# Kernel optimization log

Hardware: AMD Instinct MI355X
Metric: run time of the kernel (lower is better)

The kernel has to match this reference:

```python
import jax, jax.numpy as jnp
import numpy as np

B, A, D, H, NL, DFF, V, NB = 32, 256, 512, 8, 6, 2048, 1000, 4
EMB = D // 8  # per-subtoken embedding dim, 8 subtokens concat to d_model


def setup_inputs() -> dict:
    key = jax.random.key(0)
    ks = jax.random.split(key, 10)
    s = 0.02
    p = {}
    p["src"] = jax.random.randint(ks[0], (B, A, 8), 0, V, dtype=jnp.int32)
    p["mask"] = jnp.ones((B, 1, A), dtype=bool)
    p["max_atoms"] = A
    # sinusoidal positional encoding table [A, D]
    pos = np.arange(A, dtype=np.float32)[:, None]
    div = np.power(10000.0, np.arange(0, D, 2, dtype=np.float32) / D)
    pe = np.zeros((A, D), dtype=np.float32)
    pe[:, 0::2] = np.sin(pos / div)
    pe[:, 1::2] = np.cos(pos / div)
    p["pe"] = jnp.asarray(pe)
    p["embed"] = s * jax.random.normal(ks[1], (V, EMB), dtype=jnp.float32)
    p["Wq"] = s * jax.random.normal(ks[2], (NL, D, D), dtype=jnp.float32)
    p["Wk"] = s * jax.random.normal(ks[3], (NL, D, D), dtype=jnp.float32)
    p["Wv"] = s * jax.random.normal(ks[4], (NL, D, D), dtype=jnp.float32)
    p["Wo"] = s * jax.random.normal(ks[5], (NL, D, D), dtype=jnp.float32)
    p["W1"] = s * jax.random.normal(ks[6], (NL, D, DFF), dtype=jnp.float32)
    p["W2"] = s * jax.random.normal(ks[7], (NL, DFF, D), dtype=jnp.float32)
    p["Wfl"] = s * jax.random.normal(ks[8], (2 * D, NB), dtype=jnp.float32)
    for n, sh in [("bq", (NL, D)), ("bk", (NL, D)), ("bv", (NL, D)), ("bo", (NL, D)),
                  ("b1", (NL, DFF)), ("b2", (NL, D)), ("ln1_b", (NL, D)), ("ln2_b", (NL, D)),
                  ("fn_b", (D,)), ("bfl", (NB,))]:
        p[n] = jnp.zeros(sh, dtype=jnp.float32)
    for n, sh in [("ln1_a", (NL, D)), ("ln2_a", (NL, D)), ("fn_a", (D,))]:
        p[n] = jnp.ones(sh, dtype=jnp.float32)
    return p


def _norm(x, a, b):
    # custom Norm: alpha * (x - mean) / (std_unbiased + eps) + bias
    mu = x.mean(-1, keepdims=True)
    sd = jnp.std(x, axis=-1, ddof=1, keepdims=True)
    return a * (x - mu) / (sd + 1e-6) + b


def _forward(src, mask, max_atoms, embed, pe, Wq, bq, Wk, bk, Wv, bv, Wo, bo,
             ln1_a, ln1_b, ln2_a, ln2_b, W1, b1, W2, b2, fn_a, fn_b, Wfl, bfl):
    b, L = src.shape[0], src.shape[1]
    x = embed[src].reshape(b, L, -1)  # [B, A, D]
    d = x.shape[-1]
    x = x * jnp.sqrt(jnp.float32(d)) + pe[None, :L]
    dk = d // H
    addm = jnp.where(mask[:, None, :, :], 0.0, -1e9)  # [B,1,1,A]
    for i in range(NL):
        # pre-norm self-attention + residual
        x2 = _norm(x, ln1_a[i], ln1_b[i])
        q = (x2 @ Wq[i] + bq[i]).reshape(b, L, H, dk)
        k = (x2 @ Wk[i] + bk[i]).reshape(b, L, H, dk)
        v = (x2 @ Wv[i] + bv[i]).reshape(b, L, H, dk)
        sc = jnp.einsum('bqhd,bkhd->bhqk', q, k) / jnp.sqrt(jnp.float32(dk)) + addm
        att = jax.nn.softmax(sc, axis=-1)
        o = jnp.einsum('bhqk,bkhd->bqhd', att, v).reshape(b, L, d)
        x = x + (o @ Wo[i] + bo[i])
        # pre-norm FFN + residual
        x2 = _norm(x, ln2_a[i], ln2_b[i])
        x = x + (jax.nn.relu(x2 @ W1[i] + b1[i]) @ W2[i] + b2[i])
    h = _norm(x, fn_a, fn_b)  # [B, A, D]
    # EdgeClassify: all-pairs concat(h_i, h_j) @ Wfl + bfl, computed without
    # materializing the [B, A, A, 2D] tensor (linearity of the Linear layer)
    left = h @ Wfl[:d]    # [B, A, NB]
    right = h @ Wfl[d:]   # [B, A, NB]
    return left[:, :, None, :] + right[:, None, :, :] + bfl  # [B, A, A, NB]


def reference(src, mask, max_atoms, pe, embed, Wq, Wk, Wv, Wo, W1, W2, Wfl,
              bq, bk, bv, bo, b1, b2, ln1_b, ln2_b, fn_b, bfl, ln1_a, ln2_a, fn_a):
    return _forward(src, mask, max_atoms, embed, pe, Wq, bq, Wk, bk, Wv, bv, Wo, bo,
                    ln1_a, ln1_b, ln2_a, ln2_b, W1, b1, W2, b2, fn_a, fn_b, Wfl, bfl)
```

## Files before the change

kernel.cpp:

```cpp
#include <hip/hip_runtime.h>
#include <hip/hip_bf16.h>
#include <type_traits>

#define BB 32
#define AA 256
#define DD 512
#define HH 8
#define NLAYER 6
#define DFF 2048
#define NB 4

typedef float  f32x4_t  __attribute__((ext_vector_type(4)));
typedef short  bf16x8_t __attribute__((ext_vector_type(8)));

struct __align__(16) US8 { ushort u[8]; };

__device__ __forceinline__ ushort f2bf(float f) {
    __hip_bfloat16 h = __float2bfloat16(f);
    return *reinterpret_cast<ushort*>(&h);
}
__device__ __forceinline__ float bf2f(ushort u) {
    __hip_bfloat16 h;
    *reinterpret_cast<ushort*>(&h) = u;
    return __bfloat162float(h);
}

__device__ __forceinline__ void gload16(const void* g, void* l) {
    __builtin_amdgcn_global_load_lds(
        (const __attribute__((address_space(1))) void*)g,
        (__attribute__((address_space(3))) void*)l, 16, 0, 0);
}

template<int N> __device__ __forceinline__ void wait_vmcnt() {
    if constexpr      (N == 0)  asm volatile("s_waitcnt vmcnt(0)"  ::: "memory");
    else if constexpr (N == 3)  asm volatile("s_waitcnt vmcnt(3)"  ::: "memory");
    else if constexpr (N == 4)  asm volatile("s_waitcnt vmcnt(4)"  ::: "memory");
    else static_assert(N == 0, "add vmcnt literal");
}
template<int N> using ic = std::integral_constant<int, N>;

__global__ __launch_bounds__(256) void embed_pe_kernel(
    const int* __restrict__ src, const float* __restrict__ embed,
    const float* __restrict__ pe, float* __restrict__ x)
{
    int t = blockIdx.x * 256 + threadIdx.x;
    int d4 = t & 127;
    int row = t >> 7;
    int a = row & 255;
    int d = d4 * 4;
    int sub = d >> 6;
    int e = d & 63;
    int tok = src[row * 8 + sub];
    float4 em = *(const float4*)&embed[tok * 64 + e];
    float4 p  = *(const float4*)&pe[a * DD + d];
    const float s = 22.627416997969522f;
    float4 r;
    r.x = em.x * s + p.x; r.y = em.y * s + p.y;
    r.z = em.z * s + p.z; r.w = em.w * s + p.w;
    *(float4*)&x[(long long)row * DD + d] = r;
}

template<bool OB>
__global__ __launch_bounds__(256) void layernorm512_kernel(
    const float* x, const float* __restrict__ alpha,
    const float* __restrict__ beta, void* yv)
{
    const int row = blockIdx.x * 4 + (threadIdx.x >> 6);
    const int lane = threadIdx.x & 63;
    const float* xr = x + (long long)row * DD;
    float4 v0 = *(const float4*)&xr[lane * 8];
    float4 v1 = *(const float4*)&xr[lane * 8 + 4];
    float s  = v0.x + v0.y + v0.z + v0.w + v1.x + v1.y + v1.z + v1.w;
    float ss = v0.x*v0.x + v0.y*v0.y + v0.z*v0.z + v0.w*v0.w
             + v1.x*v1.x + v1.y*v1.y + v1.z*v1.z + v1.w*v1.w;
    #pragma unroll
    for (int off = 1; off < 64; off <<= 1) {
        s  += __shfl_xor(s, off, 64);
        ss += __shfl_xor(ss, off, 64);
    }
    float mu = s * (1.0f / 512.0f);
    float var = fmaxf(ss - 512.0f * mu * mu, 0.0f) * (1.0f / 511.0f);
    float inv = 1.0f / (sqrtf(var) + 1e-6f);
    float4 a0 = *(const float4*)&alpha[lane * 8];
    float4 a1 = *(const float4*)&alpha[lane * 8 + 4];
    float4 b0 = *(const float4*)&beta[lane * 8];
    float4 b1 = *(const float4*)&beta[lane * 8 + 4];
    float o0 = a0.x * (v0.x - mu) * inv + b0.x;
    float o1 = a0.y * (v0.y - mu) * inv + b0.y;
    float o2 = a0.z * (v0.z - mu) * inv + b0.z;
    float o3 = a0.w * (v0.w - mu) * inv + b0.w;
    float o4 = a1.x * (v1.x - mu) * inv + b1.x;
    float o5 = a1.y * (v1.y - mu) * inv + b1.y;
    float o6 = a1.z * (v1.z - mu) * inv + b1.z;
    float o7 = a1.w * (v1.w - mu) * inv + b1.w;
    if (OB) {
        US8 o;
        o.u[0] = f2bf(o0); o.u[1] = f2bf(o1); o.u[2] = f2bf(o2); o.u[3] = f2bf(o3);
        o.u[4] = f2bf(o4); o.u[5] = f2bf(o5); o.u[6] = f2bf(o6); o.u[7] = f2bf(o7);
        *(US8*)((ushort*)yv + (long long)row * DD + lane * 8) = o;
    } else {
        float* yr = (float*)yv + (long long)row * DD + lane * 8;
        float4 w0 = {o0, o1, o2, o3}, w1 = {o4, o5, o6, o7};
        *(float4*)yr = w0;
        *(float4*)(yr + 4) = w1;
    }
}

__global__ __launch_bounds__(256) void wtrans_kernel(
    const float* __restrict__ src, ushort* __restrict__ dst,
    int Nsz, int Ksz, long long sSrc, long long sDst)
{
    __shared__ float tile[64][65];
    src += blockIdx.z * sSrc;
    dst += blockIdx.z * sDst;
    const int n0 = blockIdx.x * 64, k0 = blockIdx.y * 64;
    const int t = threadIdx.x, col = t & 63, r4 = t >> 6;
    #pragma unroll
    for (int p = 0; p < 16; ++p) {
        int row = p * 4 + r4;
        tile[row][col] = src[(long long)(k0 + row) * Nsz + n0 + col];
    }
    __syncthreads();
    #pragma unroll
    for (int p = 0; p < 16; ++p) {
        int row = p * 4 + r4;
        dst[(long long)(n0 + row) * Ksz + k0 + col] = f2bf(tile[col][row]);
    }
}

__global__ __launch_bounds__(256) void vtrans_kernel(
    const ushort* __restrict__ qkv, ushort* __restrict__ vT)
{
    __shared__ ushort tile[64][65];
    const int b = blockIdx.z;
    const int c0 = blockIdx.x * 64, a0 = blockIdx.y * 64;
    const int t = threadIdx.x, col = t & 63, r4 = t >> 6;
    const ushort* src = qkv + (long long)b * 256 * 1536 + 1024;
    ushort* dst = vT + (long long)b * 512 * 256;
    #pragma unroll
    for (int p = 0; p < 16; ++p) {
        int row = p * 4 + r4;
        tile[row][col] = src[(long long)(a0 + row) * 1536 + c0 + col];
    }
    __syncthreads();
    #pragma unroll
    for (int p = 0; p < 16; ++p) {
        int row = p * 4 + r4;
        dst[(long long)(c0 + row) * 256 + a0 + col] = tile[col][row];
    }
}

__global__ void concat_bias_kernel(const float* __restrict__ bq,
    const float* __restrict__ bk, const float* __restrict__ bv,
    float* __restrict__ o)
{
    int i = blockIdx.x * 256 + threadIdx.x;
    if (i >= NLAYER * 1536) return;
    int l = i / 1536, r = i % 1536;
    float v = r < 512 ? bq[l * 512 + r]
            : (r < 1024 ? bk[l * 512 + r - 512] : bv[l * 512 + r - 1024]);
    o[i] = v;
}

__global__ __launch_bounds__(512, 1) void attn_kernel(
    const ushort* __restrict__ qkv, const ushort* __restrict__ vT,
    ushort* __restrict__ Ob)
{
    __shared__ ushort Kl[256 * 64];
    __shared__ ushort Vl[64 * 256];
    __shared__ ushort Pl[8 * 16 * 256];

    const int t = threadIdx.x;
    const int bh = blockIdx.x;
    const int b = bh >> 3, h = bh & 7;
    const int w = t >> 6, lane = t & 63;
    const int lr = lane & 15, lg = lane >> 4;

    {
        const int j = t >> 3, slot = t & 7;
        const int chunk = slot ^ (j & 7);
        const ushort* srcK = qkv + (long long)(b * 256 + j) * 1536 + 512 + h * 64 + chunk * 8;
        const int c = t >> 5, slv = t & 31;
        const int chv = slv ^ (c & 7);
        const ushort* srcV = vT + (long long)b * 131072 + (long long)(h * 64 + c) * 256 + chv * 8;
        #pragma unroll
        for (int r = 0; r < 4; ++r) {
            gload16(srcK + (long long)r * 64 * 1536, &Kl[(t + r * 512) * 8]);
            gload16(srcV + (long long)r * 16 * 256,  &Vl[(t + r * 512) * 8]);
        }
    }
    asm volatile("s_waitcnt vmcnt(0)" ::: "memory");
    __builtin_amdgcn_sched_barrier(0);
    __builtin_amdgcn_s_barrier();
    __builtin_amdgcn_sched_barrier(0);

    char* Pw = (char*)Pl + w * 8192;
    const char* Kc = (const char*)Kl;
    const char* Vc = (const char*)Vl;

    #pragma unroll 1
    for (int pass = 0; pass < 2; ++pass) {
        const int i0 = pass * 128 + w * 16;
        const ushort* qbase = qkv + (long long)(b * 256 + i0 + lr) * 1536 + h * 64 + lg * 8;
        bf16x8_t qf0 = *(const bf16x8_t*)qbase;
        bf16x8_t qf1 = *(const bf16x8_t*)(qbase + 32);

        f32x4_t s[16];
        #pragma unroll
        for (int jf = 0; jf < 16; ++jf) s[jf] = (f32x4_t){0.f, 0.f, 0.f, 0.f};
        #pragma unroll
        for (int jf = 0; jf < 16; ++jf) {
            const int row = jf * 16 + lr;
            bf16x8_t k0 = *(const bf16x8_t*)(Kc + row * 128 + ((lg ^ (row & 7)) * 16));
            s[jf] = __builtin_amdgcn_mfma_f32_16x16x32_bf16(k0, qf0, s[jf], 0, 0, 0);
        }
        #pragma unroll
        for (int jf = 0; jf < 16; ++jf) {
            const int row = jf * 16 + lr;
            bf16x8_t k1 = *(const bf16x8_t*)(Kc + row * 128 + (((4 + lg) ^ (row & 7)) * 16));
            s[jf] = __builtin_amdgcn_mfma_f32_16x16x32_bf16(k1, qf1, s[jf], 0, 0, 0);
        }

        float m = -3.0e38f;
        #pragma unroll
        for (int jf = 0; jf < 16; ++jf)
            #pragma unroll
            for (int r = 0; r < 4; ++r) m = fmaxf(m, s[jf][r]);
        m = fmaxf(m, __shfl_xor(m, 16, 64));
        m = fmaxf(m, __shfl_xor(m, 32, 64));
        float l = 0.f;
        #pragma unroll
        for (int jf = 0; jf < 16; ++jf)
            #pragma unroll
            for (int r = 0; r < 4; ++r) {
                float e = __expf((s[jf][r] - m) * 0.125f);
                s[jf][r] = e; l += e;
            }
        l += __shfl_xor(l, 16, 64);
        l += __shfl_xor(l, 32, 64);
        const float inv = 1.0f / l;

        #pragma unroll
        for (int jf = 0; jf < 16; ++jf) {
            ushort4 u;
            u.x = f2bf(s[jf][0] * inv); u.y = f2bf(s[jf][1] * inv);
            u.z = f2bf(s[jf][2] * inv); u.w = f2bf(s[jf][3] * inv);
            const int off = (lr * 512 + jf * 32 + lg * 8) ^ ((lr & 7) << 4);
            *(ushort4*)(Pw + off) = u;
        }
        asm volatile("s_waitcnt lgkmcnt(0)" ::: "memory");
        __builtin_amdgcn_sched_barrier(0);

        f32x4_t o[4];
        #pragma unroll
        for (int cf = 0; cf < 4; ++cf) o[cf] = (f32x4_t){0.f, 0.f, 0.f, 0.f};
        #pragma unroll
        for (int ks = 0; ks < 8; ++ks) {
            bf16x8_t pa = *(const bf16x8_t*)(Pw +
                ((lr * 512 + ks * 64 + lg * 16) ^ ((lr & 7) << 4)));
            #pragma unroll
            for (int cf = 0; cf < 4; ++cf) {
                const int crow = cf * 16 + lr;
                bf16x8_t vb = *(const bf16x8_t*)(Vc + crow * 512 +
                    (((ks * 4 + lg) ^ (crow & 7)) * 16));
                o[cf] = __builtin_amdgcn_mfma_f32_16x16x32_bf16(pa, vb, o[cf], 0, 0, 0);
            }
        }
        asm volatile("s_waitcnt lgkmcnt(0)" ::: "memory");
        __builtin_amdgcn_sched_barrier(0);

        #pragma unroll
        for (int cf = 0; cf < 4; ++cf) {
            const int c = cf * 16 + lr;
            #pragma unroll
            for (int r = 0; r < 4; ++r) {
                const int i = i0 + lg * 4 + r;
                Ob[(long long)(b * 256 + i) * 512 + h * 64 + c] = f2bf(o[cf][r]);
            }
        }
    }
}

template<int NT, bool RELU>
__global__ __launch_bounds__(512) void gemm_wide(
    const ushort* __restrict__ A, const ushort* __restrict__ B,
    const float* __restrict__ bias, ushort* __restrict__ C,
    int lda, int ldb, int ldc, int gn)
{
    constexpr int BK = 32;
    constexpr int S = 3;
    __shared__ ushort As[3][256 * BK];
    __shared__ ushort Bs[3][128 * BK];

    const int t = threadIdx.x;
    const int nwg = gridDim.x, bid = blockIdx.x;
    const int swz = (bid & 7) * (nwg >> 3) + (bid >> 3);
    const int nb = swz % gn;
    const int mb = swz / gn;
    const int m0 = mb * 256, n0 = nb * 128;

    const int trow  = t >> 2;
    const int tslot = (t & 3) ^ ((t >> 3) & 3);
    const ushort* Ap = A + (long long)(m0 + trow) * lda + tslot * 8;
    const ushort* Bp = B + (long long)(n0 + trow) * ldb + tslot * 8;

    const int w = t >> 6, lane = t & 63;
    const int wr = w >> 1, wc = w & 1;
    const int lr = lane & 15;
    const int slotK = (((lane >> 4) ^ ((lr >> 1) & 3)) * 8);

    f32x4_t acc[4][4];
    #pragma unroll
    for (int i = 0; i < 4; ++i)
        #pragma unroll
        for (int j = 0; j < 4; ++j)
            acc[i][j] = (f32x4_t){0.f, 0.f, 0.f, 0.f};

    auto stage = [&](int pf) {
        const int buf = pf % 3;
        const long long ko = (long long)pf * BK;
        gload16(Ap + ko,                        &As[buf][t * 8]);
        gload16(Ap + ko + (long long)128 * lda, &As[buf][t * 8 + 4096]);
        gload16(Bp + ko,                        &Bs[buf][t * 8]);
    };

    auto kstep = [&](auto wn, int kt, int pf) {
        wait_vmcnt<decltype(wn)::value>();
        __builtin_amdgcn_sched_barrier(0);
        __builtin_amdgcn_s_barrier();
        __builtin_amdgcn_sched_barrier(0);
        if (pf >= 0) stage(pf);
        __builtin_amdgcn_sched_barrier(0);
        const int cb = kt % 3;
        bf16x8_t af[4], bfr[4];
        #pragma unroll
        for (int mf = 0; mf < 4; ++mf)
            af[mf] = *(const bf16x8_t*)&As[cb][(wr * 64 + mf * 16 + lr) * BK + slotK];
        #pragma unroll
        for (int nf = 0; nf < 4; ++nf)
            bfr[nf] = *(const bf16x8_t*)&Bs[cb][(wc * 64 + nf * 16 + lr) * BK + slotK];
        __builtin_amdgcn_s_setprio(1);
        #pragma unroll
        for (int mf = 0; mf < 4; ++mf)
            #pragma unroll
            for (int nf = 0; nf < 4; ++nf)
                acc[mf][nf] = __builtin_amdgcn_mfma_f32_16x16x32_bf16(
                    af[mf], bfr[nf], acc[mf][nf], 0, 0, 0);
        __builtin_amdgcn_s_setprio(0);
    };

    stage(0);
    stage(1);
    for (int kt = 0; kt < NT - 1; ++kt)
        kstep(ic<S>{}, kt, (kt + 2 < NT) ? (kt + 2) : -1);
    kstep(ic<0>{}, NT - 1, -1);

    #pragma unroll
    for (int nf = 0; nf < 4; ++nf) {
        const int col = n0 + wc * 64 + nf * 16 + lr;
        const float bv = bias[col];
        #pragma unroll
        for (int mf = 0; mf < 4; ++mf) {
            const int row0 = m0 + wr * 64 + mf * 16 + (lane >> 4) * 4;
            #pragma unroll
            for (int j = 0; j < 4; ++j) {
                float vv = acc[mf][nf][j] + bv;
                if (RELU) vv = fmaxf(vv, 0.0f);
                C[(long long)(row0 + j) * ldc + col] = f2bf(vv);
            }
        }
    }
}

template<int BMt, int BNt, int NT, bool OBF16, bool RELU, bool RES, bool SWZ>
__global__ __launch_bounds__(256) void gemm_nar(
    const ushort* __restrict__ A, const ushort* __restrict__ B,
    const float* __restrict__ bias, const float* __restrict__ res,
    void* __restrict__ Cv, int lda, int ldb, int ldc, int gx,
    int zdiv, long long sA1, long long sA2, long long sB1, long long sB2,
    long long sC1, long long sC2)
{
    constexpr int BK = 32;
    constexpr int AI = (BMt * BK) / 2048;
    constexpr int BI = (BNt * BK) / 2048;
    constexpr int S  = AI + BI;
    constexpr int HM = BMt / 2, HN = BNt / 2;
    constexpr int RM = HM / 16, RN = HN / 16;

    __shared__ ushort As[3][BMt * BK];
    __shared__ ushort Bs[3][BNt * BK];

    const int t = threadIdx.x;
    int nb, mb, zq, zr;
    if (SWZ) {
        const int nwg = gridDim.x, bid = blockIdx.x;
        const int swz = (bid & 7) * (nwg >> 3) + (bid >> 3);
        nb = swz % gx; mb = swz / gx; zq = 0; zr = 0;
    } else {
        nb = blockIdx.x; mb = blockIdx.y;
        const int z = blockIdx.z;
        zq = z / zdiv; zr = z % zdiv;
    }
    const int m0 = mb * BMt, n0 = nb * BNt;

    const int trow  = t >> 2;
    const int tslot = (t & 3) ^ ((t >> 3) & 3);
    const ushort* Ap = A + zq * sA1 + zr * sA2
                     + (long long)(m0 + trow) * lda + tslot * 8;
    const ushort* Bp = B + zq * sB1 + zr * sB2
                     + (long long)(n0 + trow) * ldb + tslot * 8;

    const int w = t >> 6, lane = t & 63;
    const int wr = w >> 1, wc = w & 1;
    const int lr = lane & 15;
    const int slotK = (((lane >> 4) ^ ((lr >> 1) & 3)) * 8);

    f32x4_t acc[RM][RN];
    #pragma unroll
    for (int i = 0; i < RM; ++i)
        #pragma unroll
        for (int j = 0; j < RN; ++j)
            acc[i][j] = (f32x4_t){0.f, 0.f, 0.f, 0.f};

    auto stage = [&](int pf) {
        const int buf = pf % 3;
        const long long ko = (long long)pf * BK;
        #pragma unroll
        for (int i = 0; i < AI; ++i)
            gload16(Ap + ko + (long long)i * 64 * lda, &As[buf][t * 8 + i * 2048]);
        #pragma unroll
        for (int i = 0; i < BI; ++i)
            gload16(Bp + ko + (long long)i * 64 * ldb, &Bs[buf][t * 8 + i * 2048]);
    };

    auto kstep = [&](auto wn, int kt, int pf) {
        wait_vmcnt<decltype(wn)::value>();
        __builtin_amdgcn_sched_barrier(0);
        __builtin_amdgcn_s_barrier();
        __builtin_amdgcn_sched_barrier(0);
        if (pf >= 0) stage(pf);
        __builtin_amdgcn_sched_barrier(0);
        const int cb = kt % 3;
        bf16x8_t af[RM], bfr[RN];
        #pragma unroll
        for (int mf = 0; mf < RM; ++mf)
            af[mf] = *(const bf16x8_t*)&As[cb][(wr * HM + mf * 16 + lr) * BK + slotK];
        #pragma unroll
        for (int nf = 0; nf < RN; ++nf)
            bfr[nf] = *(const bf16x8_t*)&Bs[cb][(wc * HN + nf * 16 + lr) * BK + slotK];
        __builtin_amdgcn_s_setprio(1);
        #pragma unroll
        for (int mf = 0; mf < RM; ++mf)
            #pragma unroll
            for (int nf = 0; nf < RN; ++nf)
                acc[mf][nf] = __builtin_amdgcn_mfma_f32_16x16x32_bf16(
                    af[mf], bfr[nf], acc[mf][nf], 0, 0, 0);
        __builtin_amdgcn_s_setprio(0);
    };

    stage(0);
    if constexpr (NT >= 2) stage(1);
    for (int kt = 0; kt < NT - 1; ++kt)
        kstep(ic<S>{}, kt, (kt + 2 < NT) ? (kt + 2) : -1);
    kstep(ic<0>{}, NT - 1, -1);

    const long long coff = zq * sC1 + zr * sC2;
    #pragma unroll
    for (int nf = 0; nf < RN; ++nf) {
        const int col = n0 + wc * HN + nf * 16 + lr;
        const float bv = bias ? bias[col] : 0.0f;
        #pragma unroll
        for (int mf = 0; mf < RM; ++mf) {
            const int row0 = m0 + wr * HM + mf * 16 + (lane >> 4) * 4;
            #pragma unroll
            for (int j = 0; j < 4; ++j) {
                float vv = acc[mf][nf][j] + bv;
                if (RELU) vv = fmaxf(vv, 0.0f);
                const long long idx = coff + (long long)(row0 + j) * ldc + col;
                if (RES) vv += res[idx];
                if (OBF16) ((ushort*)Cv)[idx] = f2bf(vv);
                else       ((float*)Cv)[idx]  = vv;
            }
        }
    }
}

__global__ __launch_bounds__(256) void edge_heads_kernel(
    const float* __restrict__ h, const float* __restrict__ Wfl,
    float* __restrict__ L, float* __restrict__ R)
{
    int row = blockIdx.x * 4 + (threadIdx.x >> 6);
    int lane = threadIdx.x & 63;
    const float* hr = h + (long long)row * DD;
    float accL[NB] = {}, accR[NB] = {};
    #pragma unroll
    for (int tt = 0; tt < 8; ++tt) {
        int e = lane * 8 + tt;
        float hv = hr[e];
        #pragma unroll
        for (int n = 0; n < NB; ++n) {
            accL[n] = fmaf(hv, Wfl[e * NB + n], accL[n]);
            accR[n] = fmaf(hv, Wfl[(DD + e) * NB + n], accR[n]);
        }
    }
    #pragma unroll
    for (int n = 0; n < NB; ++n) {
        #pragma unroll
        for (int off = 1; off < 64; off <<= 1) {
            accL[n] += __shfl_xor(accL[n], off, 64);
            accR[n] += __shfl_xor(accR[n], off, 64);
        }
    }
    if (lane == 0) {
        #pragma unroll
        for (int n = 0; n < NB; ++n) {
            L[row * NB + n] = accL[n];
            R[row * NB + n] = accR[n];
        }
    }
}

__global__ __launch_bounds__(256) void edge_combine_kernel(
    const float* __restrict__ L, const float* __restrict__ R,
    const float* __restrict__ bfl, float* __restrict__ out)
{
    int idx = blockIdx.x * 256 + threadIdx.x;
    int j = idx & 255;
    int bi = idx >> 8;
    int b = bi >> 8;
    float4 l = *(const float4*)&L[bi * NB];
    float4 r = *(const float4*)&R[(b * 256 + j) * NB];
    float4 bf = *(const float4*)bfl;
    float4 o;
    o.x = l.x + r.x + bf.x; o.y = l.y + r.y + bf.y;
    o.z = l.z + r.z + bf.z; o.w = l.w + r.w + bf.w;
    *(float4*)&out[(long long)idx * NB] = o;
}

extern "C" void kernel_launch(void* const* d_in, const int* in_sizes, int n_in,
                              void* d_out, int out_size, void* d_ws, size_t ws_size,
                              hipStream_t stream)
{
    const int*   src   = (const int*)  d_in[0];
    const float* pe    = (const float*)d_in[3];
    const float* emb   = (const float*)d_in[4];
    const float* Wq    = (const float*)d_in[5];
    const float* Wk    = (const float*)d_in[6];
    const float* Wv    = (const float*)d_in[7];
    const float* Wo    = (const float*)d_in[8];
    const float* W1    = (const float*)d_in[9];
    const float* W2    = (const float*)d_in[10];
    const float* Wfl   = (const float*)d_in[11];
    const float* bq    = (const float*)d_in[12];
    const float* bk    = (const float*)d_in[13];
    const float* bv    = (const float*)d_in[14];
    const float* bo    = (const float*)d_in[15];
    const float* b1    = (const float*)d_in[16];
    const float* b2    = (const float*)d_in[17];
    const float* ln1_b = (const float*)d_in[18];
    const float* ln2_b = (const float*)d_in[19];
    const float* fn_b  = (const float*)d_in[20];
    const float* bfl   = (const float*)d_in[21];
    const float* ln1_a = (const float*)d_in[22];
    const float* ln2_a = (const float*)d_in[23];
    const float* fn_a  = (const float*)d_in[24];
    float* out = (float*)d_out;

    const long long ROWS = (long long)BB * AA;
    char* p = (char*)d_ws;
    float*  x    = (float*)p;  p += ROWS * DD * 4;
    ushort* x2b  = (ushort*)p; p += ROWS * DD * 2;
    ushort* qkv  = (ushort*)p;
    ushort* h1   = qkv;
    p += ROWS * 1536 * 2;
    ushort* vT   = (ushort*)p; p += (long long)BB * DD * AA * 2;
    ushort* Wqkvt= (ushort*)p; p += (long long)NLAYER * 1536 * 512 * 2;
    ushort* Wot  = (ushort*)p; p += (long long)NLAYER * 512 * 512 * 2;
    ushort* W1t  = (ushort*)p; p += (long long)NLAYER * 2048 * 512 * 2;
    ushort* W2t  = (ushort*)p; p += (long long)NLAYER * 512 * 2048 * 2;
    float*  bqkv = (float*)p;  p += (long long)NLAYER * 1536 * 4;
    float*  left = (float*)p;  p += ROWS * NB * 4;
    float*  right= (float*)p;  p += ROWS * NB * 4;

    wtrans_kernel<<<dim3(8, 8, 6),  256, 0, stream>>>(Wq, Wqkvt,          512,  512,  262144LL,  786432LL);
    wtrans_kernel<<<dim3(8, 8, 6),  256, 0, stream>>>(Wk, Wqkvt + 262144, 512,  512,  262144LL,  786432LL);
    wtrans_kernel<<<dim3(8, 8, 6),  256, 0, stream>>>(Wv, Wqkvt + 524288, 512,  512,  262144LL,  786432LL);
    wtrans_kernel<<<dim3(8, 8, 6),  256, 0, stream>>>(Wo, Wot,            512,  512,  262144LL,  262144LL);
    wtrans_kernel<<<dim3(32, 8, 6), 256, 0, stream>>>(W1, W1t,            2048, 512,  1048576LL, 1048576LL);
    wtrans_kernel<<<dim3(8, 32, 6), 256, 0, stream>>>(W2, W2t,            512,  2048, 1048576LL, 1048576LL);
    concat_bias_kernel<<<36, 256, 0, stream>>>(bq, bk, bv, bqkv);

    embed_pe_kernel<<<4096, 256, 0, stream>>>(src, emb, pe, x);

    for (int i = 0; i < NLAYER; ++i) {
        layernorm512_kernel<true><<<2048, 256, 0, stream>>>(
            x, ln1_a + i * DD, ln1_b + i * DD, x2b);
        gemm_wide<16, false><<<384, 512, 0, stream>>>(
            x2b, Wqkvt + (long long)i * 786432, bqkv + i * 1536, qkv,
            512, 512, 1536, 12);
        vtrans_kernel<<<dim3(8, 4, 32), 256, 0, stream>>>(qkv, vT);
        attn_kernel<<<256, 512, 0, stream>>>(qkv, vT, x2b);
        gemm_nar<128, 64, 16, false, false, true, true><<<512, 256, 0, stream>>>(
            x2b, Wot + (long long)i * 262144, bo + i * DD, x, x,
            512, 512, 512, 8, 1, 0, 0, 0, 0, 0, 0);
        layernorm512_kernel<true><<<2048, 256, 0, stream>>>(
            x, ln2_a + i * DD, ln2_b + i * DD, x2b);
        gemm_wide<16, true><<<512, 512, 0, stream>>>(
            x2b, W1t + (long long)i * 1048576, b1 + i * DFF, h1,
            512, 512, 2048, 16);
        gemm_nar<128, 64, 64, false, false, true, true><<<512, 256, 0, stream>>>(
            h1, W2t + (long long)i * 1048576, b2 + i * DD, x, x,
            2048, 2048, 512, 8, 1, 0, 0, 0, 0, 0, 0);
    }

    layernorm512_kernel<false><<<2048, 256, 0, stream>>>(x, fn_a, fn_b, x);
    edge_heads_kernel<<<2048, 256, 0, stream>>>(x, Wfl, left, right);
    edge_combine_kernel<<<8192, 256, 0, stream>>>(left, right, bfl, out);
}
```

Measured before the change: 842.7 us.

## Fuse V transpose into QKV GEMM epilogue and use 128x128 tiles for wide GEMMs

Removes the separate vtrans kernel. The QKV GEMM epilogue now writes Q and K into a 1024-wide buffer and scatters V directly in transposed layout into vT. The 256x128 gemm_wide kernel is dropped, and the QKV and FFN1 GEMMs run on the generic gemm_nar with 128x128 tiles, 256 threads and more blocks. This saves one kernel launch and a round trip of V through memory per layer. In exchange, the V stores in the epilogue are strided and uncoalesced, and the different tile shape changes per-block reuse.

```diff
diff --git a/kernel.cpp b/kernel.cpp
--- a/kernel.cpp
+++ b/kernel.cpp
@@ -128,28 +128,6 @@
     }
 }
 
-__global__ __launch_bounds__(256) void vtrans_kernel(
-    const ushort* __restrict__ qkv, ushort* __restrict__ vT)
-{
-    __shared__ ushort tile[64][65];
-    const int b = blockIdx.z;
-    const int c0 = blockIdx.x * 64, a0 = blockIdx.y * 64;
-    const int t = threadIdx.x, col = t & 63, r4 = t >> 6;
-    const ushort* src = qkv + (long long)b * 256 * 1536 + 1024;
-    ushort* dst = vT + (long long)b * 512 * 256;
-    #pragma unroll
-    for (int p = 0; p < 16; ++p) {
-        int row = p * 4 + r4;
-        tile[row][col] = src[(long long)(a0 + row) * 1536 + c0 + col];
-    }
-    __syncthreads();
-    #pragma unroll
-    for (int p = 0; p < 16; ++p) {
-        int row = p * 4 + r4;
-        dst[(long long)(c0 + row) * 256 + a0 + col] = tile[col][row];
-    }
-}
-
 __global__ void concat_bias_kernel(const float* __restrict__ bq,
     const float* __restrict__ bk, const float* __restrict__ bv,
     float* __restrict__ o)
@@ -163,7 +141,7 @@
 }
 
 __global__ __launch_bounds__(512, 1) void attn_kernel(
-    const ushort* __restrict__ qkv, const ushort* __restrict__ vT,
+    const ushort* __restrict__ qk, const ushort* __restrict__ vT,
     ushort* __restrict__ Ob)
 {
     __shared__ ushort Kl[256 * 64];
@@ -179,13 +157,13 @@
     {
         const int j = t >> 3, slot = t & 7;
         const int chunk = slot ^ (j & 7);
-        const ushort* srcK = qkv + (long long)(b * 256 + j) * 1536 + 512 + h * 64 + chunk * 8;
+        const ushort* srcK = qk + (long long)(b * 256 + j) * 1024 + 512 + h * 64 + chunk * 8;
         const int c = t >> 5, slv = t & 31;
         const int chv = slv ^ (c & 7);
         const ushort* srcV = vT + (long long)b * 131072 + (long long)(h * 64 + c) * 256 + chv * 8;
         #pragma unroll
         for (int r = 0; r < 4; ++r) {
-            gload16(srcK + (long long)r * 64 * 1536, &Kl[(t + r * 512) * 8]);
+            gload16(srcK + (long long)r * 64 * 1024, &Kl[(t + r * 512) * 8]);
             gload16(srcV + (long long)r * 16 * 256,  &Vl[(t + r * 512) * 8]);
         }
     }
@@ -201,7 +179,7 @@
     #pragma unroll 1
     for (int pass = 0; pass < 2; ++pass) {
         const int i0 = pass * 128 + w * 16;
-        const ushort* qbase = qkv + (long long)(b * 256 + i0 + lr) * 1536 + h * 64 + lg * 8;
+        const ushort* qbase = qk + (long long)(b * 256 + i0 + lr) * 1024 + h * 64 + lg * 8;
         bf16x8_t qf0 = *(const bf16x8_t*)qbase;
         bf16x8_t qf1 = *(const bf16x8_t*)(qbase + 32);
 
@@ -281,104 +259,12 @@
     }
 }
 
-template<int NT, bool RELU>
-__global__ __launch_bounds__(512) void gemm_wide(
-    const ushort* __restrict__ A, const ushort* __restrict__ B,
-    const float* __restrict__ bias, ushort* __restrict__ C,
-    int lda, int ldb, int ldc, int gn)
-{
-    constexpr int BK = 32;
-    constexpr int S = 3;
-    __shared__ ushort As[3][256 * BK];
-    __shared__ ushort Bs[3][128 * BK];
-
-    const int t = threadIdx.x;
-    const int nwg = gridDim.x, bid = blockIdx.x;
-    const int swz = (bid & 7) * (nwg >> 3) + (bid >> 3);
-    const int nb = swz % gn;
-    const int mb = swz / gn;
-    const int m0 = mb * 256, n0 = nb * 128;
-
-    const int trow  = t >> 2;
-    const int tslot = (t & 3) ^ ((t >> 3) & 3);
-    const ushort* Ap = A + (long long)(m0 + trow) * lda + tslot * 8;
-    const ushort* Bp = B + (long long)(n0 + trow) * ldb + tslot * 8;
-
-    const int w = t >> 6, lane = t & 63;
-    const int wr = w >> 1, wc = w & 1;
-    const int lr = lane & 15;
-    const int slotK = (((lane >> 4) ^ ((lr >> 1) & 3)) * 8);
-
-    f32x4_t acc[4][4];
-    #pragma unroll
-    for (int i = 0; i < 4; ++i)
-        #pragma unroll
-        for (int j = 0; j < 4; ++j)
-            acc[i][j] = (f32x4_t){0.f, 0.f, 0.f, 0.f};
-
-    auto stage = [&](int pf) {
-        const int buf = pf % 3;
-        const long long ko = (long long)pf * BK;
-        gload16(Ap + ko,                        &As[buf][t * 8]);
-        gload16(Ap + ko + (long long)128 * lda, &As[buf][t * 8 + 4096]);
-        gload16(Bp + ko,                        &Bs[buf][t * 8]);
-    };
-
-    auto kstep = [&](auto wn, int kt, int pf) {
-        wait_vmcnt<decltype(wn)::value>();
-        __builtin_amdgcn_sched_barrier(0);
-        __builtin_amdgcn_s_barrier();
-        __builtin_amdgcn_sched_barrier(0);
-        if (pf >= 0) stage(pf);
-        __builtin_amdgcn_sched_barrier(0);
-        const int cb = kt % 3;
-        bf16x8_t af[4], bfr[4];
-        #pragma unroll
-        for (int mf = 0; mf < 4; ++mf)
-            af[mf] = *(const bf16x8_t*)&As[cb][(wr * 64 + mf * 16 + lr) * BK + slotK];
-        #pragma unroll
-        for (int nf = 0; nf < 4; ++nf)
-            bfr[nf] = *(const bf16x8_t*)&Bs[cb][(wc * 64 + nf * 16 + lr) * BK + slotK];
-        __builtin_amdgcn_s_setprio(1);
-        #pragma unroll
-        for (int mf = 0; mf < 4; ++mf)
-            #pragma unroll
-            for (int nf = 0; nf < 4; ++nf)
-                acc[mf][nf] = __builtin_amdgcn_mfma_f32_16x16x32_bf16(
-                    af[mf], bfr[nf], acc[mf][nf], 0, 0, 0);
-        __builtin_amdgcn_s_setprio(0);
-    };
-
-    stage(0);
-    stage(1);
-    for (int kt = 0; kt < NT - 1; ++kt)
-        kstep(ic<S>{}, kt, (kt + 2 < NT) ? (kt + 2) : -1);
-    kstep(ic<0>{}, NT - 1, -1);
-
-    #pragma unroll
-    for (int nf = 0; nf < 4; ++nf) {
-        const int col = n0 + wc * 64 + nf * 16 + lr;
-        const float bv = bias[col];
-        #pragma unroll
-        for (int mf = 0; mf < 4; ++mf) {
-            const int row0 = m0 + wr * 64 + mf * 16 + (lane >> 4) * 4;
-            #pragma unroll
-            for (int j = 0; j < 4; ++j) {
-                float vv = acc[mf][nf][j] + bv;
-                if (RELU) vv = fmaxf(vv, 0.0f);
-                C[(long long)(row0 + j) * ldc + col] = f2bf(vv);
-            }
-        }
-    }
-}
-
-template<int BMt, int BNt, int NT, bool OBF16, bool RELU, bool RES, bool SWZ>
+template<int BMt, int BNt, int NT, int OUT, bool RELU, bool SWZ>
 __global__ __launch_bounds__(256) void gemm_nar(
     const ushort* __restrict__ A, const ushort* __restrict__ B,
     const float* __restrict__ bias, const float* __restrict__ res,
-    void* __restrict__ Cv, int lda, int ldb, int ldc, int gx,
-    int zdiv, long long sA1, long long sA2, long long sB1, long long sB2,
-    long long sC1, long long sC2)
+    void* __restrict__ Cv, ushort* __restrict__ C2,
+    int lda, int ldb, int ldc, int gx)
 {
     constexpr int BK = 32;
     constexpr int AI = (BMt * BK) / 2048;
@@ -391,24 +277,20 @@
     __shared__ ushort Bs[3][BNt * BK];
 
     const int t = threadIdx.x;
-    int nb, mb, zq, zr;
+    int nb, mb;
     if (SWZ) {
         const int nwg = gridDim.x, bid = blockIdx.x;
         const int swz = (bid & 7) * (nwg >> 3) + (bid >> 3);
-        nb = swz % gx; mb = swz / gx; zq = 0; zr = 0;
+        nb = swz % gx; mb = swz / gx;
     } else {
         nb = blockIdx.x; mb = blockIdx.y;
-        const int z = blockIdx.z;
-        zq = z / zdiv; zr = z % zdiv;
     }
     const int m0 = mb * BMt, n0 = nb * BNt;
 
     const int trow  = t >> 2;
     const int tslot = (t & 3) ^ ((t >> 3) & 3);
-    const ushort* Ap = A + zq * sA1 + zr * sA2
-                     + (long long)(m0 + trow) * lda + tslot * 8;
-    const ushort* Bp = B + zq * sB1 + zr * sB2
-                     + (long long)(n0 + trow) * ldb + tslot * 8;
+    const ushort* Ap = A + (long long)(m0 + trow) * lda + tslot * 8;
+    const ushort* Bp = B + (long long)(n0 + trow) * ldb + tslot * 8;
 
     const int w = t >> 6, lane = t & 63;
     const int wr = w >> 1, wc = w & 1;
@@ -459,16 +341,15 @@
     };
 
     stage(0);
-    if constexpr (NT >= 2) stage(1);
+    stage(1);
     for (int kt = 0; kt < NT - 1; ++kt)
         kstep(ic<S>{}, kt, (kt + 2 < NT) ? (kt + 2) : -1);
     kstep(ic<0>{}, NT - 1, -1);
 
-    const long long coff = zq * sC1 + zr * sC2;
     #pragma unroll
     for (int nf = 0; nf < RN; ++nf) {
         const int col = n0 + wc * HN + nf * 16 + lr;
-        const float bv = bias ? bias[col] : 0.0f;
+        const float bv = bias[col];
         #pragma unroll
         for (int mf = 0; mf < RM; ++mf) {
             const int row0 = m0 + wr * HM + mf * 16 + (lane >> 4) * 4;
@@ -476,10 +357,20 @@
             for (int j = 0; j < 4; ++j) {
                 float vv = acc[mf][nf][j] + bv;
                 if (RELU) vv = fmaxf(vv, 0.0f);
-                const long long idx = coff + (long long)(row0 + j) * ldc + col;
-                if (RES) vv += res[idx];
-                if (OBF16) ((ushort*)Cv)[idx] = f2bf(vv);
-                else       ((float*)Cv)[idx]  = vv;
+                const int row = row0 + j;
+                if (OUT == 0) {
+                    ((ushort*)Cv)[(long long)row * ldc + col] = f2bf(vv);
+                } else if (OUT == 1) {
+                    const long long idx = (long long)row * ldc + col;
+                    ((float*)Cv)[idx] = vv + res[idx];
+                } else {
+                    if (col < 1024) {
+                        ((ushort*)Cv)[(long long)row * 1024 + col] = f2bf(vv);
+                    } else {
+                        const int bq_ = row >> 8, a_ = row & 255;
+                        C2[(long long)bq_ * 131072 + (long long)(col - 1024) * 256 + a_] = f2bf(vv);
+                    }
+                }
             }
         }
     }
@@ -570,10 +461,11 @@
     char* p = (char*)d_ws;
     float*  x    = (float*)p;  p += ROWS * DD * 4;
     ushort* x2b  = (ushort*)p; p += ROWS * DD * 2;
-    ushort* qkv  = (ushort*)p;
-    ushort* h1   = qkv;
-    p += ROWS * 1536 * 2;
+    ushort* qk   = (ushort*)p;
+    ushort* h1   = qk;
+    p += ROWS * 1024 * 2;
     ushort* vT   = (ushort*)p; p += (long long)BB * DD * AA * 2;
+    p += 8 * 1024 * 1024;
     ushort* Wqkvt= (ushort*)p; p += (long long)NLAYER * 1536 * 512 * 2;
     ushort* Wot  = (ushort*)p; p += (long long)NLAYER * 512 * 512 * 2;
     ushort* W1t  = (ushort*)p; p += (long long)NLAYER * 2048 * 512 * 2;
@@ -595,22 +487,21 @@
     for (int i = 0; i < NLAYER; ++i) {
         layernorm512_kernel<true><<<2048, 256, 0, stream>>>(
             x, ln1_a + i * DD, ln1_b + i * DD, x2b);
-        gemm_wide<16, false><<<384, 512, 0, stream>>>(
-            x2b, Wqkvt + (long long)i * 786432, bqkv + i * 1536, qkv,
-            512, 512, 1536, 12);
-        vtrans_kernel<<<dim3(8, 4, 32), 256, 0, stream>>>(qkv, vT);
-        attn_kernel<<<256, 512, 0, stream>>>(qkv, vT, x2b);
-        gemm_nar<128, 64, 16, false, false, true, true><<<512, 256, 0, stream>>>(
-            x2b, Wot + (long long)i * 262144, bo + i * DD, x, x,
-            512, 512, 512, 8, 1, 0, 0, 0, 0, 0, 0);
+        gemm_nar<128, 128, 16, 2, false, true><<<768, 256, 0, stream>>>(
+            x2b, Wqkvt + (long long)i * 786432, bqkv + i * 1536, nullptr,
+            qk, vT, 512, 512, 1024, 12);
+        attn_kernel<<<256, 512, 0, stream>>>(qk, vT, x2b);
+        gemm_nar<128, 64, 16, 1, false, true><<<512, 256, 0, stream>>>(
+            x2b, Wot + (long long)i * 262144, bo + i * DD, x,
+            x, nullptr, 512, 512, 512, 8);
         layernorm512_kernel<true><<<2048, 256, 0, stream>>>(
             x, ln2_a + i * DD, ln2_b + i * DD, x2b);
-        gemm_wide<16, true><<<512, 512, 0, stream>>>(
-            x2b, W1t + (long long)i * 1048576, b1 + i * DFF, h1,
-            512, 512, 2048, 16);
-        gemm_nar<128, 64, 64, false, false, true, true><<<512, 256, 0, stream>>>(
-            h1, W2t + (long long)i * 1048576, b2 + i * DD, x, x,
-            2048, 2048, 512, 8, 1, 0, 0, 0, 0, 0, 0);
+        gemm_nar<128, 128, 16, 0, true, true><<<1024, 256, 0, stream>>>(
+            x2b, W1t + (long long)i * 1048576, b1 + i * DFF, nullptr,
+            h1, nullptr, 512, 512, 2048, 16);
+        gemm_nar<128, 64, 64, 1, false, true><<<512, 256, 0, stream>>>(
+            h1, W2t + (long long)i * 1048576, b2 + i * DD, x,
+            x, nullptr, 2048, 2048, 512, 8);
     }
 
     layernorm512_kernel<false><<<2048, 256, 0, stream>>>(x, fn_a, fn_b, x);
```

Result: no change. 836.2 us (-0.8%).
